# Optimization experiments

Hardware: AMD Instinct MI355X
Metric: run time of the kernel (lower is better)

Reference implementation:

```python
import jax, jax.numpy as jnp
import numpy as np

BETA = 0.9      # LIF leak
THRESH = 1.0    # snntorch Leaky default threshold
SLOPE = 25.0    # fast_sigmoid surrogate slope

@jax.custom_vjp
def spike(x):
    # Heaviside forward, fast_sigmoid surrogate backward
    return (x > 0).astype(x.dtype)

def _spike_fwd(x):
    return spike(x), x

def _spike_bwd(x, g):
    return (g / (SLOPE * jnp.abs(x) + 1.0) ** 2,)

spike.defvjp(_spike_fwd, _spike_bwd)


def setup_inputs() -> dict:
    key = jax.random.key(0)
    k0, k1, k2, k3, k4 = jax.random.split(key, 5)
    B, T, I, H, C = 256, 100, 512, 1024, 8
    x = jax.random.normal(k0, (B, T, I), dtype=jnp.float32)
    s1 = 1.0 / np.sqrt(I)
    s2 = 1.0 / np.sqrt(H)
    W1 = jax.random.uniform(k1, (H, I), jnp.float32, -s1, s1)
    b1 = jax.random.uniform(k2, (H,), jnp.float32, -s1, s1)
    W2 = jax.random.uniform(k3, (C, H), jnp.float32, -s2, s2)
    b2 = jax.random.uniform(k4, (C,), jnp.float32, -s2, s2)
    return {"x": x, "W1": W1, "b1": b1, "W2": W2, "b2": b2}


def reference(x, W1, b1, W2, b2):
    # x: [B, T, I]
    B, T, I = x.shape
    H = W1.shape[0]
    # fc1 for all timesteps as one big GEMM (same math as per-step loop).
    cur = jnp.einsum('bti,hi->tbh', x, W1) + b1  # [T, B, H]

    def step(mem, c):
        # snntorch Leaky (reset_mechanism='subtract'):
        reset = spike(mem - THRESH)
        mem_new = BETA * mem + c - reset * THRESH
        spk = spike(mem_new - THRESH)
        return mem_new, spk

    mem0 = jnp.zeros((B, H), dtype=x.dtype)
    _, spk_rec = jax.lax.scan(step, mem0, cur)  # spk_rec: [T, B, H]

    # sum_t (spk_t @ W2.T + b2) == (sum_t spk_t) @ W2.T + T*b2
    spk_sum = spk_rec.sum(axis=0)  # [B, H]
    logits = spk_sum @ W2.T + T * b2  # [B, C]
    return logits
```

## Files before the change

kernel.cpp:

```cpp
#include <hip/hip_runtime.h>


#define B_   256
#define T_   100
#define I_   512
#define H_   1024
#define C_   8
#define M_   (B_ * T_)
#define KS_  1024
#define SC   64.0f
#define ISC  (1.0f / 4096.0f)
#define CP   132

typedef _Float16 half8 __attribute__((ext_vector_type(8)));
typedef _Float16 half4 __attribute__((ext_vector_type(4)));
typedef float floatx4 __attribute__((ext_vector_type(4)));

__device__ __forceinline__ void ld_g2l(const _Float16* g, _Float16* l) {
    __builtin_amdgcn_global_load_lds(
        (const __attribute__((address_space(1))) void*)g,
        (__attribute__((address_space(3))) void*)l, 16, 0, 0);
}

__global__ void __launch_bounds__(256)
split_x(const float* __restrict__ x, _Float16* __restrict__ A) {
    int g = blockIdx.x * 256 + threadIdx.x;
    int i0 = (g & 127) * 4;
    int m = g >> 7;
    float4 v = *(const float4*)(x + (size_t)m * I_ + i0);
    float vv[4] = {v.x, v.y, v.z, v.w};
    half4 hi, lo;
#pragma unroll
    for (int j = 0; j < 4; ++j) {
        float s = vv[j] * SC;
        _Float16 h = (_Float16)s;
        hi[j] = h;
        lo[j] = (_Float16)(s - (float)h);
    }
    _Float16* r = A + (size_t)m * KS_ + i0;
    *(half4*)(r) = hi;
    *(half4*)(r + 512) = lo;
}

__global__ void __launch_bounds__(256)
split_w_init(const float* __restrict__ w, _Float16* __restrict__ Wp,
             const float* __restrict__ b2, float* __restrict__ out) {
    int g = blockIdx.x * 256 + threadIdx.x;
    if (g < B_ * C_) out[g] = 100.0f * b2[g & (C_ - 1)];
    int i0 = (g & 127) * 4;
    int h = g >> 7;
    float4 v = *(const float4*)(w + (size_t)h * I_ + i0);
    float vv[4] = {v.x, v.y, v.z, v.w};
    half4 hi, lo;
#pragma unroll
    for (int j = 0; j < 4; ++j) {
        float s = vv[j] * SC;
        _Float16 hh = (_Float16)s;
        hi[j] = hh;
        lo[j] = (_Float16)(s - (float)hh);
    }
    _Float16* r = Wp + (size_t)h * KS_ + i0;
    *(half4*)(r) = hi;
    *(half4*)(r + 512) = lo;
}

__global__ void __launch_bounds__(256, 4)
snn_mfma(const _Float16* __restrict__ Asp, const _Float16* __restrict__ Wsp,
         const float* __restrict__ b1, const float* __restrict__ W2,
         float* __restrict__ logits) {
    __shared__ union {
        struct { __align__(16) _Float16 A[128 * 64]; __align__(16) _Float16 Bm[128 * 64]; } g;
        float Cs[64 * CP];
    } sm;
    const int tid = threadIdx.x;
    const int lane = tid & 63;
    const int w = tid >> 6;

    const int xcd = blockIdx.x & 7;
    const int jj = blockIdx.x >> 3;
    const int b  = xcd * 32 + (jj >> 3);
    const int n0 = (jj & 7) * 128;

    const int wm = (w >> 1) * 64;
    const int wn = (w & 1) * 64;
    const int srow = lane >> 3;
    const int sc16 = (lane & 7) ^ srow;

    const _Float16* ag[4];
    const _Float16* bg[4];
    _Float16* al[4];
    _Float16* bl[4];
#pragma unroll
    for (int j = 0; j < 4; ++j) {
        const int r = w * 32 + j * 8 + srow;
        ag[j] = Asp + ((size_t)b * T_ + r) * KS_ + sc16 * 8;
        bg[j] = Wsp + (size_t)(n0 + r) * KS_ + sc16 * 8;
        al[j] = &sm.g.A[(w * 32 + j * 8) * 64];
        bl[j] = &sm.g.Bm[(w * 32 + j * 8) * 64];
    }

    floatx4 acc[4][4];
#pragma unroll
    for (int i = 0; i < 4; ++i)
#pragma unroll
        for (int q = 0; q < 4; ++q) acc[i][q] = (floatx4){0.f, 0.f, 0.f, 0.f};

    const int quad = lane >> 4;
    const int l15 = lane & 15;
    const int l7 = lane & 7;

    for (int kt = 0; kt < 24; ++kt) {
        const int koA = ((kt & 16) ? 512 : 0) + (kt & 7) * 64;
        const int koB = ((kt & 8)  ? 512 : 0) + (kt & 7) * 64;
        __syncthreads();
#pragma unroll
        for (int j = 0; j < 4; ++j) {
            ld_g2l(ag[j] + koA, al[j]);
            ld_g2l(bg[j] + koB, bl[j]);
        }
        __syncthreads();
#pragma unroll
        for (int ks = 0; ks < 2; ++ks) {
            half8 av[4], bv[4];
#pragma unroll
            for (int f = 0; f < 4; ++f) {
                const int c16 = (ks * 4 + quad) ^ l7;
                av[f] = *(const half8*)&sm.g.A[(wm + f * 16 + l15) * 64 + c16 * 8];
                bv[f] = *(const half8*)&sm.g.Bm[(wn + f * 16 + l15) * 64 + c16 * 8];
            }
#pragma unroll
            for (int fr = 0; fr < 4; ++fr)
#pragma unroll
                for (int fn = 0; fn < 4; ++fn)
                    acc[fr][fn] = __builtin_amdgcn_mfma_f32_16x16x32_f16(
                        av[fr], bv[fn], acc[fr][fn], 0, 0, 0);
        }
    }

    float b1c[4];
#pragma unroll
    for (int fn = 0; fn < 4; ++fn) b1c[fn] = b1[n0 + wn + fn * 16 + l15];

    float mem = 0.f, ss = 0.f;
    const int myh = tid & 127;

    __syncthreads();
    if (w < 2) {
#pragma unroll
        for (int fr = 0; fr < 4; ++fr)
#pragma unroll
            for (int r = 0; r < 4; ++r) {
                float* dst = &sm.Cs[(fr * 16 + quad * 4 + r) * CP + wn + l15];
#pragma unroll
                for (int fn = 0; fn < 4; ++fn)
                    dst[fn * 16] = acc[fr][fn][r] * ISC + b1c[fn];
            }
    }
    __syncthreads();
    if (tid < 128) {
#pragma unroll 8
        for (int t = 0; t < 64; ++t) {
            float c = sm.Cs[t * CP + myh];
            float reset = (mem > 1.0f) ? 1.0f : 0.0f;
            mem = 0.9f * mem + c - reset;
            ss += (mem > 1.0f) ? 1.0f : 0.0f;
        }
    }
    __syncthreads();
    if (w >= 2) {
#pragma unroll
        for (int fr = 0; fr < 4; ++fr)
#pragma unroll
            for (int r = 0; r < 4; ++r) {
                float* dst = &sm.Cs[(fr * 16 + quad * 4 + r) * CP + wn + l15];
#pragma unroll
                for (int fn = 0; fn < 4; ++fn)
                    dst[fn * 16] = acc[fr][fn][r] * ISC + b1c[fn];
            }
    }
    __syncthreads();
    if (tid < 128) {
#pragma unroll 6
        for (int t = 0; t < 36; ++t) {
            float c = sm.Cs[t * CP + myh];
            float reset = (mem > 1.0f) ? 1.0f : 0.0f;
            mem = 0.9f * mem + c - reset;
            ss += (mem > 1.0f) ? 1.0f : 0.0f;
        }
#pragma unroll
        for (int c = 0; c < C_; ++c) {
            float v = ss * W2[c * H_ + n0 + myh];
#pragma unroll
            for (int off = 32; off; off >>= 1) v += __shfl_down(v, off, 64);
            if (lane == 0) atomicAdd(&logits[b * C_ + c], v);
        }
    }
}

extern "C" void kernel_launch(void* const* d_in, const int* in_sizes, int n_in,
                              void* d_out, int out_size, void* d_ws, size_t ws_size,
                              hipStream_t stream) {
    const float* x  = (const float*)d_in[0];
    const float* W1 = (const float*)d_in[1];
    const float* b1 = (const float*)d_in[2];
    const float* W2 = (const float*)d_in[3];
    const float* b2 = (const float*)d_in[4];
    float* out = (float*)d_out;

    char* ws = (char*)d_ws;
    _Float16* Asp = (_Float16*)ws;
    _Float16* Wsp = (_Float16*)(ws + (size_t)M_ * KS_ * 2);

    hipLaunchKernelGGL(split_x, dim3(M_ * 128 / 256), dim3(256), 0, stream, x, Asp);
    hipLaunchKernelGGL(split_w_init, dim3(H_ * 128 / 256), dim3(256), 0, stream,
                       W1, Wsp, b2, out);
    hipLaunchKernelGGL(snn_mfma, dim3(B_ * 8), dim3(256), 0, stream,
                       Asp, Wsp, b1, W2, out);
}
```

Measured before the change: 210.0 us.

## Merge split kernels and skip padding rows beyond T in the GEMM tile

Folds the x and W1 fp16 hi/lo split into one launch with 8-wide vector stores, and relies on Wsp sitting directly after Asp. In the MFMA kernel, the 128-row A tile covers 100 timesteps, so the fourth wave skips loading the last 16 padding rows. The bottom warps drop their fourth fragment row except for the 48-63 slice, and the second epilogue stores only 3 fragment rows. This cuts wasted MFMA work and loads on rows past T and removes one launch, at the cost of more divergent control flow in the inner loop.

```diff
diff --git a/kernel.cpp b/kernel.cpp
--- a/kernel.cpp
+++ b/kernel.cpp
@@ -13,7 +13,6 @@
 #define CP   132
 
 typedef _Float16 half8 __attribute__((ext_vector_type(8)));
-typedef _Float16 half4 __attribute__((ext_vector_type(4)));
 typedef float floatx4 __attribute__((ext_vector_type(4)));
 
 __device__ __forceinline__ void ld_g2l(const _Float16* g, _Float16* l) {
@@ -23,45 +22,29 @@
 }
 
 __global__ void __launch_bounds__(256)
-split_x(const float* __restrict__ x, _Float16* __restrict__ A) {
+split_all(const float* __restrict__ x, const float* __restrict__ W1,
+          const float* __restrict__ b2, _Float16* __restrict__ Asp,
+          float* __restrict__ out) {
     int g = blockIdx.x * 256 + threadIdx.x;
-    int i0 = (g & 127) * 4;
-    int m = g >> 7;
-    float4 v = *(const float4*)(x + (size_t)m * I_ + i0);
-    float vv[4] = {v.x, v.y, v.z, v.w};
-    half4 hi, lo;
-#pragma unroll
-    for (int j = 0; j < 4; ++j) {
+    if (g < B_ * C_) out[g] = 100.0f * b2[g & (C_ - 1)];
+    int row = g >> 6;
+    int i0 = (g & 63) * 8;
+    const float* src = (row < M_) ? (x + (size_t)row * I_ + i0)
+                                  : (W1 + (size_t)(row - M_) * I_ + i0);
+    float4 v0 = *(const float4*)(src);
+    float4 v1 = *(const float4*)(src + 4);
+    float vv[8] = {v0.x, v0.y, v0.z, v0.w, v1.x, v1.y, v1.z, v1.w};
+    half8 hi, lo;
+#pragma unroll
+    for (int j = 0; j < 8; ++j) {
         float s = vv[j] * SC;
         _Float16 h = (_Float16)s;
         hi[j] = h;
         lo[j] = (_Float16)(s - (float)h);
     }
-    _Float16* r = A + (size_t)m * KS_ + i0;
-    *(half4*)(r) = hi;
-    *(half4*)(r + 512) = lo;
-}
-
-__global__ void __launch_bounds__(256)
-split_w_init(const float* __restrict__ w, _Float16* __restrict__ Wp,
-             const float* __restrict__ b2, float* __restrict__ out) {
-    int g = blockIdx.x * 256 + threadIdx.x;
-    if (g < B_ * C_) out[g] = 100.0f * b2[g & (C_ - 1)];
-    int i0 = (g & 127) * 4;
-    int h = g >> 7;
-    float4 v = *(const float4*)(w + (size_t)h * I_ + i0);
-    float vv[4] = {v.x, v.y, v.z, v.w};
-    half4 hi, lo;
-#pragma unroll
-    for (int j = 0; j < 4; ++j) {
-        float s = vv[j] * SC;
-        _Float16 hh = (_Float16)s;
-        hi[j] = hh;
-        lo[j] = (_Float16)(s - (float)hh);
-    }
-    _Float16* r = Wp + (size_t)h * KS_ + i0;
-    *(half4*)(r) = hi;
-    *(half4*)(r + 512) = lo;
+    _Float16* r = Asp + (size_t)row * KS_ + i0;
+    *(half8*)(r) = hi;
+    *(half8*)(r + 512) = lo;
 }
 
 __global__ void __launch_bounds__(256, 4)
@@ -115,25 +98,33 @@
         __syncthreads();
 #pragma unroll
         for (int j = 0; j < 4; ++j) {
-            ld_g2l(ag[j] + koA, al[j]);
+            if (j < 2 || w < 3) ld_g2l(ag[j] + koA, al[j]);
             ld_g2l(bg[j] + koB, bl[j]);
         }
         __syncthreads();
 #pragma unroll
         for (int ks = 0; ks < 2; ++ks) {
-            half8 av[4], bv[4];
-#pragma unroll
-            for (int f = 0; f < 4; ++f) {
-                const int c16 = (ks * 4 + quad) ^ l7;
+            const int c16 = (ks * 4 + quad) ^ l7;
+            half8 av[3], bv[4];
+#pragma unroll
+            for (int f = 0; f < 3; ++f)
                 av[f] = *(const half8*)&sm.g.A[(wm + f * 16 + l15) * 64 + c16 * 8];
+#pragma unroll
+            for (int f = 0; f < 4; ++f)
                 bv[f] = *(const half8*)&sm.g.Bm[(wn + f * 16 + l15) * 64 + c16 * 8];
-            }
-#pragma unroll
-            for (int fr = 0; fr < 4; ++fr)
+#pragma unroll
+            for (int fr = 0; fr < 3; ++fr)
 #pragma unroll
                 for (int fn = 0; fn < 4; ++fn)
                     acc[fr][fn] = __builtin_amdgcn_mfma_f32_16x16x32_f16(
                         av[fr], bv[fn], acc[fr][fn], 0, 0, 0);
+            if (wm == 0) {
+                half8 a3 = *(const half8*)&sm.g.A[(48 + l15) * 64 + c16 * 8];
+#pragma unroll
+                for (int fn = 0; fn < 4; ++fn)
+                    acc[3][fn] = __builtin_amdgcn_mfma_f32_16x16x32_f16(
+                        a3, bv[fn], acc[3][fn], 0, 0, 0);
+            }
         }
     }
 
@@ -169,7 +160,7 @@
     __syncthreads();
     if (w >= 2) {
 #pragma unroll
-        for (int fr = 0; fr < 4; ++fr)
+        for (int fr = 0; fr < 3; ++fr)
 #pragma unroll
             for (int r = 0; r < 4; ++r) {
                 float* dst = &sm.Cs[(fr * 16 + quad * 4 + r) * CP + wn + l15];
@@ -211,9 +202,8 @@
     _Float16* Asp = (_Float16*)ws;
     _Float16* Wsp = (_Float16*)(ws + (size_t)M_ * KS_ * 2);
 
-    hipLaunchKernelGGL(split_x, dim3(M_ * 128 / 256), dim3(256), 0, stream, x, Asp);
-    hipLaunchKernelGGL(split_w_init, dim3(H_ * 128 / 256), dim3(256), 0, stream,
-                       W1, Wsp, b2, out);
+    hipLaunchKernelGGL(split_all, dim3((M_ + H_) * 64 / 256), dim3(256), 0, stream,
+                       x, W1, b2, Asp, out);
     hipLaunchKernelGGL(snn_mfma, dim3(B_ * 8), dim3(256), 0, stream,
                        Asp, Wsp, b1, W2, out);
 }
```

Measured after the change: 195.2 us. -7.1%, faster.
